# Performance work log

Hardware: AMD Instinct MI355X
Metric: run time of the kernel (lower is better)

The kernel has to match this reference:

```python
import jax, jax.numpy as jnp
import numpy as np

N_OSC = 256
N_LAYERS = 4
STEPS = 10
DT = 0.1
B = 1024
D_IN = 512
D_OUT = 128


def setup_inputs() -> dict:
    key = jax.random.key(0)
    ks = jax.random.split(key, 12)
    n = N_OSC

    def rn(k, shape, s=1.0):
        return jax.random.normal(k, shape, jnp.float32) * s

    K = rn(ks[0], (N_LAYERS, n, n), 0.1)
    K = (K + jnp.swapaxes(K, -1, -2)) / 2  # symmetric init as in torch
    return {
        "x": rn(ks[1], (B, D_IN)),
        "enc_W1": rn(ks[2], (D_IN, 2 * n), 0.02), "enc_b1": jnp.zeros((2 * n,), jnp.float32),
        "enc_W2": rn(ks[3], (2 * n, n), 0.02), "enc_b2": jnp.zeros((n,), jnp.float32),
        "K": K,
        "omega": rn(ks[4], (N_LAYERS, n), 0.1),
        "K_global": jnp.full((N_LAYERS,), 0.5, jnp.float32),
        "op_strength": jnp.full((6,), 0.5, jnp.float32),
        "exchange_logits": rn(ks[5], (n, n), 0.1),
        "catalyze_freq": rn(ks[6], (n,), 0.1),
        "sel_W1": rn(ks[7], (n + 2, 64), 0.05), "sel_b1": jnp.zeros((64,), jnp.float32),
        "sel_W2": rn(ks[8], (64, 6), 0.05), "sel_b2": jnp.zeros((6,), jnp.float32),
        "dec_W1": rn(ks[9], (2 * n, 2 * D_OUT), 0.02), "dec_b1": jnp.zeros((2 * D_OUT,), jnp.float32),
        "dec_W2": rn(ks[10], (2 * D_OUT, D_OUT), 0.02), "dec_b2": jnp.zeros((D_OUT,), jnp.float32),
        "z_momentum": jnp.float32(0.1),
        "z_decay": jnp.float32(0.05),
    }


def _kuramoto_layer(theta, K, omega, K_global):
    n = theta.shape[-1]

    def step(th, _):
        diff = th[:, None, :] - th[:, :, None]          # [B, i, j] = theta_j - theta_i
        coupling = jnp.sum(K * jnp.sin(diff), axis=-1)  # reduce over j -> [B, n]
        th_new = th + DT * (omega + (K_global / n) * coupling)
        th_new = jnp.arctan2(jnp.sin(th_new), jnp.cos(th_new))  # wrap to (-pi, pi]
        return th_new, None

    theta, _ = jax.lax.scan(jax.checkpoint(step), theta, None, length=STEPS)
    cm = jnp.mean(jnp.cos(theta), axis=-1)
    sm = jnp.mean(jnp.sin(theta), axis=-1)
    return theta, jnp.sqrt(cm * cm + sm * sm)  # Kuramoto order parameter r


def _soft_permutation(logits):
    P = logits
    for _ in range(5):  # Sinkhorn normalization in log space
        P = P - jax.nn.logsumexp(P, axis=-1, keepdims=True)
        P = P - jax.nn.logsumexp(P, axis=-2, keepdims=True)
    return jnp.exp(P)


def _forward(x, enc_W1, enc_b1, enc_W2, enc_b2, K, omega, K_global,
             op_strength, exchange_logits, catalyze_freq,
             sel_W1, sel_b1, sel_W2, sel_b2, dec_W1, dec_b1, dec_W2, dec_b2,
             z_momentum, z_decay):
    n = N_OSC
    # input encoding -> initial phases in (-pi, pi)
    h = jax.nn.gelu(x @ enc_W1 + enc_b1, approximate=False)
    theta = jnp.tanh(h @ enc_W2 + enc_b2) * jnp.pi

    z = jnp.float32(0.1)
    P = _soft_permutation(exchange_logits)
    k_mult = jnp.float32(1.0)              # AMPLIFY/CONTAIN carry to next layer
    om_add = jnp.zeros((n,), theta.dtype)  # CATALYZE carry to next layer

    for li in range(N_LAYERS):
        theta, r = _kuramoto_layer(theta, K[li] * k_mult, omega[li] + om_add, K_global[li])
        # z-coordinate attractor update: dz = mom*(r_mean - z) - decay*(z - 0.5)
        dz = z_momentum * (jnp.mean(r) - z) - z_decay * (z - 0.5)
        z = jnp.clip(z + 0.01 * dz, 0.0, 1.0)
        # APL operator selection from [theta, coherence, z]
        feat = jnp.concatenate(
            [theta, r[:, None], jnp.broadcast_to(z, (theta.shape[0], 1))], axis=-1)
        logits = jax.nn.gelu(feat @ sel_W1 + sel_b1, approximate=False) @ sel_W2 + sel_b2
        op = jnp.argmax(jnp.mean(logits, axis=0))
        strength = op_strength[op] * r[:, None]  # coherence-modulated strength
        sm_ = jnp.mean(strength)
        # apply operator: phase mods now, K/omega mods carried into next layer
        noise = jax.random.normal(jax.random.fold_in(jax.random.key(42), li),
                                  theta.shape, theta.dtype)
        theta = jnp.where(op == 3, theta @ P,                                # EXCHANGE
                          jnp.where(op == 4, theta + noise * strength * 0.2,  # INHIBIT
                                    theta))
        k_mult = jnp.where(op == 1, 1.0 + sm_ * 0.5,        # AMPLIFY
                           jnp.where(op == 2, 1.0 - sm_ * 0.3, 1.0))  # CONTAIN
        om_add = jnp.where(op == 5, catalyze_freq * sm_,    # CATALYZE
                           jnp.zeros_like(catalyze_freq))

    # decode from (cos, sin) phase embedding
    emb = jnp.concatenate([jnp.cos(theta), jnp.sin(theta)], axis=-1)  # [B, 2n]
    out = jax.nn.gelu(emb @ dec_W1 + dec_b1, approximate=False) @ dec_W2 + dec_b2
    return out


def reference(x, enc_W1, enc_b1, enc_W2, enc_b2, K, omega, K_global,
              op_strength, exchange_logits, catalyze_freq,
              sel_W1, sel_b1, sel_W2, sel_b2, dec_W1, dec_b1, dec_W2, dec_b2,
              z_momentum, z_decay):
    return _forward(x, enc_W1, enc_b1, enc_W2, enc_b2, K, omega, K_global,
                    op_strength, exchange_logits, catalyze_freq,
                    sel_W1, sel_b1, sel_W2, sel_b2, dec_W1, dec_b1, dec_W2, dec_b2,
                    z_momentum, z_decay)
```

## Files before the change

kernel.cpp:

```cpp
#include <hip/hip_runtime.h>
#include <hip/hip_fp16.h>
#include <math.h>

#define DT_F 0.1f

#define SC_Z     0
#define SC_RMEAN 1
#define SC_KMULT 2
#define SC_OP    3
#define SC_OPSTR 4
#define SC_SM    5

typedef __attribute__((ext_vector_type(8))) short short8;
typedef __attribute__((ext_vector_type(4))) float f32x4;


__device__ __forceinline__ float gelu_f(float x) {
    return 0.5f * x * (1.0f + erff(x * 0.7071067811865475f));
}

__device__ __forceinline__ unsigned short f2bf_rne(float f) {
    union { float f; unsigned u; } v; v.f = f;
    unsigned x = v.u;
    unsigned r = x + 0x7fffu + ((x >> 16) & 1u);
    return (unsigned short)(r >> 16);
}

__device__ __forceinline__ unsigned rotl32(unsigned v, int d) {
    return (v << d) | (v >> (32 - d));
}

__device__ __forceinline__ void threefry2x32(unsigned k0, unsigned k1,
                                             unsigned x0, unsigned x1,
                                             unsigned& o0, unsigned& o1) {
    unsigned k2 = k0 ^ k1 ^ 0x1BD11BDAu;
    x0 += k0; x1 += k1;
    const int r0[4] = {13, 15, 26, 6};
    const int r1[4] = {17, 29, 16, 24};
#pragma unroll
    for (int g = 0; g < 5; ++g) {
        const int* R = (g & 1) ? r1 : r0;
#pragma unroll
        for (int q = 0; q < 4; ++q) { x0 += x1; x1 = rotl32(x1, R[q]); x1 ^= x0; }
        unsigned a, b;
        switch (g) {
            case 0:  a = k1; b = k2 + 1u; break;
            case 1:  a = k2; b = k0 + 2u; break;
            case 2:  a = k0; b = k1 + 3u; break;
            case 3:  a = k1; b = k2 + 4u; break;
            default: a = k2; b = k0 + 5u; break;
        }
        x0 += a; x1 += b;
    }
    o0 = x0; o1 = x1;
}

__device__ __forceinline__ float erfinv_xla(float x) {
    float w = -log1pf(-x * x);
    float p;
    if (w < 5.0f) {
        w -= 2.5f;
        p = 2.81022636e-08f;
        p = fmaf(p, w, 3.43273939e-07f);
        p = fmaf(p, w, -3.5233877e-06f);
        p = fmaf(p, w, -4.39150654e-06f);
        p = fmaf(p, w, 0.00021858087f);
        p = fmaf(p, w, -0.00125372503f);
        p = fmaf(p, w, -0.00417768164f);
        p = fmaf(p, w, 0.246640727f);
        p = fmaf(p, w, 1.50140941f);
    } else {
        w = sqrtf(w) - 3.0f;
        p = -0.000200214257f;
        p = fmaf(p, w, 0.000100950558f);
        p = fmaf(p, w, 0.00134934322f);
        p = fmaf(p, w, -0.00367342844f);
        p = fmaf(p, w, 0.00573950773f);
        p = fmaf(p, w, -0.0076224613f);
        p = fmaf(p, w, 0.00943887047f);
        p = fmaf(p, w, 1.00167406f);
        p = fmaf(p, w, 2.83297682f);
    }
    return p * x;
}

__device__ __forceinline__ float jax_normal_elem(unsigned fk0, unsigned fk1, unsigned flat) {
    const unsigned HALF = 131072u;
    unsigned idx = (flat < HALF) ? flat : (flat - HALF);
    unsigned o0, o1;
    threefry2x32(fk0, fk1, idx, idx + HALF, o0, o1);
    unsigned bits = (flat < HALF) ? o0 : o1;
    float f = __uint_as_float((bits >> 9) | 0x3F800000u) - 1.0f;
    const float LO = __uint_as_float(0xBF7FFFFFu);
    float u = fmaxf(LO, fmaf(f, 2.0f, LO));
    return 1.41421356237f * erfinv_xla(u);
}


__global__ __launch_bounds__(256) void prep_wt_kernel(
    const float* __restrict__ W1, const float* __restrict__ W2,
    const float* __restrict__ W3, const float* __restrict__ W4,
    unsigned short* __restrict__ T1, unsigned short* __restrict__ T2,
    unsigned short* __restrict__ T3, unsigned short* __restrict__ T4)
{
    __shared__ float tile[64][65];
    int b = blockIdx.x;
    const float* W; unsigned short* T; int K, N, kt, nt;
    if (b < 64)       { W = W1; T = T1; K = 512; N = 512; kt = b >> 3; nt = b & 7; }
    else if (b < 96)  { b -= 64;  W = W2; T = T2; K = 512; N = 256; kt = b >> 2; nt = b & 3; }
    else if (b < 128) { b -= 96;  W = W3; T = T3; K = 512; N = 256; kt = b >> 2; nt = b & 3; }
    else              { b -= 128; W = W4; T = T4; K = 256; N = 128; kt = b >> 1; nt = b & 1; }
    const int k0 = kt * 64, n0 = nt * 64;
    const int t = threadIdx.x;

#pragma unroll
    for (int i = 0; i < 4; ++i) {
        int r = (t >> 4) + i * 16;
        int c = (t & 15) * 4;
        float4 v = *reinterpret_cast<const float4*>(&W[(k0 + r) * N + n0 + c]);
        tile[r][c] = v.x; tile[r][c + 1] = v.y; tile[r][c + 2] = v.z; tile[r][c + 3] = v.w;
    }
    __syncthreads();
#pragma unroll
    for (int i = 0; i < 4; ++i) {
        int nn = (t >> 4) + i * 16;
        int kc = (t & 15) * 4;
        ushort4 o;
        o.x = f2bf_rne(tile[kc + 0][nn]);
        o.y = f2bf_rne(tile[kc + 1][nn]);
        o.z = f2bf_rne(tile[kc + 2][nn]);
        o.w = f2bf_rne(tile[kc + 3][nn]);
        *reinterpret_cast<ushort4*>(&T[(n0 + nn) * K + k0 + kc]) = o;
    }
}


template <int ACT, int KF, bool EMB>
__global__ __launch_bounds__(256) void gemm_mfma_kernel(
    const float* __restrict__ A,
    const unsigned short* __restrict__ Wt,
    const float* __restrict__ bias,
    float* __restrict__ C, int N)
{
    constexpr int STR = KF + 8;
    __shared__ __align__(16) unsigned short A_s[64 * STR];
    __shared__ __align__(16) unsigned short B_s[64 * STR];
    const int tid = threadIdx.x;
    const int m_base = blockIdx.y * 64;
    const int n_base = blockIdx.x * 64;

    {
        constexpr int ITERS = 64 * KF / 2048;
#pragma unroll
        for (int c = 0; c < ITERS; ++c) {
            const int f = c * 2048 + tid * 8;
            const int row = f / KF, k = f % KF;
            float4 a0, a1;
            if (EMB) {
                const int kk = k & 255;
                a0 = *reinterpret_cast<const float4*>(&A[(m_base + row) * 256 + kk]);
                a1 = *reinterpret_cast<const float4*>(&A[(m_base + row) * 256 + kk + 4]);
                if (k < 256) {
                    a0.x = __cosf(a0.x); a0.y = __cosf(a0.y); a0.z = __cosf(a0.z); a0.w = __cosf(a0.w);
                    a1.x = __cosf(a1.x); a1.y = __cosf(a1.y); a1.z = __cosf(a1.z); a1.w = __cosf(a1.w);
                } else {
                    a0.x = __sinf(a0.x); a0.y = __sinf(a0.y); a0.z = __sinf(a0.z); a0.w = __sinf(a0.w);
                    a1.x = __sinf(a1.x); a1.y = __sinf(a1.y); a1.z = __sinf(a1.z); a1.w = __sinf(a1.w);
                }
            } else {
                a0 = *reinterpret_cast<const float4*>(&A[(m_base + row) * KF + k]);
                a1 = *reinterpret_cast<const float4*>(&A[(m_base + row) * KF + k + 4]);
            }
            short8 v;
            v[0] = (short)f2bf_rne(a0.x); v[1] = (short)f2bf_rne(a0.y);
            v[2] = (short)f2bf_rne(a0.z); v[3] = (short)f2bf_rne(a0.w);
            v[4] = (short)f2bf_rne(a1.x); v[5] = (short)f2bf_rne(a1.y);
            v[6] = (short)f2bf_rne(a1.z); v[7] = (short)f2bf_rne(a1.w);
            *reinterpret_cast<short8*>(&A_s[row * STR + k]) = v;
        }
    }
    {
        constexpr int ITERS = 64 * KF / 2048;
#pragma unroll
        for (int c = 0; c < ITERS; ++c) {
            const int f = c * 2048 + tid * 8;
            const int n = f / KF, k = f % KF;
            short8 v = *reinterpret_cast<const short8*>(&Wt[(n_base + n) * KF + k]);
            *reinterpret_cast<short8*>(&B_s[n * STR + k]) = v;
        }
    }
    __syncthreads();

    const int l = tid & 63, w = tid >> 6;
    const int lo = l & 15, hi = l >> 4;

    f32x4 acc0 = {0.f, 0.f, 0.f, 0.f};
    f32x4 acc1 = {0.f, 0.f, 0.f, 0.f};
    f32x4 acc2 = {0.f, 0.f, 0.f, 0.f};
    f32x4 acc3 = {0.f, 0.f, 0.f, 0.f};
#pragma unroll
    for (int kc = 0; kc < KF / 32; ++kc) {
        short8 af = *reinterpret_cast<const short8*>(&A_s[(w * 16 + lo) * STR + kc * 32 + hi * 8]);
        short8 b0 = *reinterpret_cast<const short8*>(&B_s[(0 * 16 + lo) * STR + kc * 32 + hi * 8]);
        short8 b1 = *reinterpret_cast<const short8*>(&B_s[(1 * 16 + lo) * STR + kc * 32 + hi * 8]);
        short8 b2 = *reinterpret_cast<const short8*>(&B_s[(2 * 16 + lo) * STR + kc * 32 + hi * 8]);
        short8 b3 = *reinterpret_cast<const short8*>(&B_s[(3 * 16 + lo) * STR + kc * 32 + hi * 8]);
        acc0 = __builtin_amdgcn_mfma_f32_16x16x32_bf16(af, b0, acc0, 0, 0, 0);
        acc1 = __builtin_amdgcn_mfma_f32_16x16x32_bf16(af, b1, acc1, 0, 0, 0);
        acc2 = __builtin_amdgcn_mfma_f32_16x16x32_bf16(af, b2, acc2, 0, 0, 0);
        acc3 = __builtin_amdgcn_mfma_f32_16x16x32_bf16(af, b3, acc3, 0, 0, 0);
    }

#pragma unroll
    for (int nf = 0; nf < 4; ++nf) {
        const f32x4 a = (nf == 0) ? acc0 : (nf == 1) ? acc1 : (nf == 2) ? acc2 : acc3;
        const int n = n_base + nf * 16 + lo;
        const float bv = bias[n];
#pragma unroll
        for (int q = 0; q < 4; ++q) {
            const int m = m_base + w * 16 + hi * 4 + q;
            float v = a[q] + bv;
            if (ACT == 1) v = gelu_f(v);
            else if (ACT == 2) v = tanhf(v) * 3.14159274101257324f;
            C[m * N + n] = v;
        }
    }
}


__global__ __launch_bounds__(1024) void sinkhorn_kernel(const float* __restrict__ logits,
                                                        float* __restrict__ P,
                                                        float* __restrict__ scal,
                                                        float* __restrict__ om_add) {
    __shared__ __align__(16) __half Eh[256][260];
    __shared__ float a[256], b[256];
    __shared__ float part[8][256];
    const int t = threadIdx.x;

    if (t < 8) {
        float val = 0.0f;
        if (t == SC_Z) val = 0.1f;
        if (t == SC_KMULT) val = 1.0f;
        scal[t] = val;
    }
    if (t < 256) { om_add[t] = 0.0f; b[t] = 1.0f; }

    {
        const int r = t >> 2, c0 = (t & 3) * 64;
#pragma unroll
        for (int j = 0; j < 64; j += 4) {
            float4 x4 = *reinterpret_cast<const float4*>(&logits[r * 256 + c0 + j]);
            __half2 h01 = __floats2half2_rn(__expf(x4.x), __expf(x4.y));
            __half2 h23 = __floats2half2_rn(__expf(x4.z), __expf(x4.w));
            *reinterpret_cast<__half2*>(&Eh[r][c0 + j])     = h01;
            *reinterpret_cast<__half2*>(&Eh[r][c0 + j + 2]) = h23;
        }
    }
    __syncthreads();

    for (int it = 0; it < 5; ++it) {
        {
            const int i = t & 255, q = t >> 8;
            float s0 = 0.f, s1 = 0.f, s2 = 0.f, s3 = 0.f;
#pragma unroll
            for (int j0 = 0; j0 < 64; j0 += 4) {
                float2 e4 = *reinterpret_cast<const float2*>(&Eh[i][q * 64 + j0]);
                const __half2* hp = reinterpret_cast<const __half2*>(&e4);
                float2 f01 = __half22float2(hp[0]);
                float2 f23 = __half22float2(hp[1]);
                float4 bv = *reinterpret_cast<const float4*>(&b[q * 64 + j0]);
                s0 = fmaf(f01.x, bv.x, s0);
                s1 = fmaf(f01.y, bv.y, s1);
                s2 = fmaf(f23.x, bv.z, s2);
                s3 = fmaf(f23.y, bv.w, s3);
            }
            part[q][i] = (s0 + s1) + (s2 + s3);
        }
        __syncthreads();
        if (t < 256) a[t] = 1.0f / (part[0][t] + part[1][t] + part[2][t] + part[3][t]);
        __syncthreads();
        {
            const int jp = t & 127, seg = t >> 7;
            float s0 = 0.f, s1 = 0.f;
#pragma unroll
            for (int i0 = 0; i0 < 32; i0 += 4) {
                float4 av = *reinterpret_cast<const float4*>(&a[seg * 32 + i0]);
                __half2 e0 = *reinterpret_cast<const __half2*>(&Eh[seg * 32 + i0 + 0][2 * jp]);
                __half2 e1 = *reinterpret_cast<const __half2*>(&Eh[seg * 32 + i0 + 1][2 * jp]);
                __half2 e2 = *reinterpret_cast<const __half2*>(&Eh[seg * 32 + i0 + 2][2 * jp]);
                __half2 e3 = *reinterpret_cast<const __half2*>(&Eh[seg * 32 + i0 + 3][2 * jp]);
                float2 f0 = __half22float2(e0), f1 = __half22float2(e1);
                float2 f2 = __half22float2(e2), f3 = __half22float2(e3);
                s0 = fmaf(f0.x, av.x, s0); s1 = fmaf(f0.y, av.x, s1);
                s0 = fmaf(f1.x, av.y, s0); s1 = fmaf(f1.y, av.y, s1);
                s0 = fmaf(f2.x, av.z, s0); s1 = fmaf(f2.y, av.z, s1);
                s0 = fmaf(f3.x, av.w, s0); s1 = fmaf(f3.y, av.w, s1);
            }
            part[seg][2 * jp]     = s0;
            part[seg][2 * jp + 1] = s1;
        }
        __syncthreads();
        if (t < 256) {
            float s = ((part[0][t] + part[1][t]) + (part[2][t] + part[3][t]))
                    + ((part[4][t] + part[5][t]) + (part[6][t] + part[7][t]));
            b[t] = 1.0f / s;
        }
        __syncthreads();
    }

    {
        const int r = t >> 2, c0 = (t & 3) * 64;
        const float ar = a[r];
#pragma unroll
        for (int j = 0; j < 64; j += 4) {
            float2 e4 = *reinterpret_cast<const float2*>(&Eh[r][c0 + j]);
            const __half2* hp = reinterpret_cast<const __half2*>(&e4);
            float2 f01 = __half22float2(hp[0]);
            float2 f23 = __half22float2(hp[1]);
            float4 bv = *reinterpret_cast<const float4*>(&b[c0 + j]);
            float4 o;
            o.x = f01.x * ar * bv.x;
            o.y = f01.y * ar * bv.y;
            o.z = f23.x * ar * bv.z;
            o.w = f23.y * ar * bv.w;
            *reinterpret_cast<float4*>(&P[r * 256 + c0 + j]) = o;
        }
    }
}


__global__ __launch_bounds__(512) void kuramoto_mfma_kernel(
    float* __restrict__ theta,
    const float* __restrict__ Kl,
    const float* __restrict__ omega_l,
    const float* __restrict__ Kg_p,
    const float* __restrict__ scal,
    const float* __restrict__ om_add,
    float* __restrict__ r_out,
    float* __restrict__ rpart,
    const float* __restrict__ P,
    int li)
{
    __shared__ __align__(16) unsigned short s_lds[2][16][264];
    __shared__ __align__(16) unsigned short c_lds[2][16][264];
    __shared__ __align__(16) float th_lds[16][260];
    __shared__ float rp_s[16][128];
    __shared__ float rp_c[16][128];
    __shared__ float red_s[16][32];
    __shared__ float red_c[16][32];
    __shared__ float rloc[16];

    const int tid = threadIdx.x;
    const int l  = tid & 63;
    const int w  = tid >> 6;
    const int lo = l & 15;
    const int hi = l >> 4;
    const int cb = w * 32;
    const int r0 = blockIdx.x * 16;

    const float gk = Kg_p[0] * (1.0f / 256.0f) * scal[SC_KMULT];
    const int op_prev = (int)scal[SC_OP];

    {
        const int row = tid >> 5;
        const int c0 = (tid & 31) * 8;
        float4 a = *reinterpret_cast<const float4*>(&theta[(r0 + row) * 256 + c0]);
        float4 b = *reinterpret_cast<const float4*>(&theta[(r0 + row) * 256 + c0 + 4]);
        *reinterpret_cast<float4*>(&th_lds[row][c0])     = a;
        *reinterpret_cast<float4*>(&th_lds[row][c0 + 4]) = b;
    }

    short8 kfrag[8][2];
#pragma unroll
    for (int nf = 0; nf < 2; ++nf) {
        const int col = cb + nf * 16 + lo;
        const float* krow = Kl + col * 256;
#pragma unroll
        for (int ks = 0; ks < 8; ++ks) {
            const int kb = ks * 32 + hi * 8;
            float4 k0 = *reinterpret_cast<const float4*>(&krow[kb]);
            float4 k1 = *reinterpret_cast<const float4*>(&krow[kb + 4]);
            short8 f;
            f[0] = (short)f2bf_rne(k0.x); f[1] = (short)f2bf_rne(k0.y);
            f[2] = (short)f2bf_rne(k0.z); f[3] = (short)f2bf_rne(k0.w);
            f[4] = (short)f2bf_rne(k1.x); f[5] = (short)f2bf_rne(k1.y);
            f[6] = (short)f2bf_rne(k1.z); f[7] = (short)f2bf_rne(k1.w);
            kfrag[ks][nf] = f;
        }
    }
    __syncthreads();

    float t[2][4];
    if (op_prev == 3) {
        float acc[2][4] = {};
        for (int j = 0; j < 256; ++j) {
            float p0 = P[j * 256 + cb + lo];
            float p1 = P[j * 256 + cb + 16 + lo];
#pragma unroll
            for (int q = 0; q < 4; ++q) {
                float tv = th_lds[hi * 4 + q][j];
                acc[0][q] = fmaf(tv, p0, acc[0][q]);
                acc[1][q] = fmaf(tv, p1, acc[1][q]);
            }
        }
#pragma unroll
        for (int nf = 0; nf < 2; ++nf)
#pragma unroll
            for (int q = 0; q < 4; ++q) t[nf][q] = acc[nf][q];
    } else {
#pragma unroll
        for (int nf = 0; nf < 2; ++nf)
#pragma unroll
            for (int q = 0; q < 4; ++q)
                t[nf][q] = th_lds[hi * 4 + q][cb + nf * 16 + lo];
        if (op_prev == 4) {
            unsigned fk0, fk1;
            threefry2x32(0u, 42u, 0u, (unsigned)(li - 1), fk0, fk1);
            const float opv = scal[SC_OPSTR];
#pragma unroll
            for (int nf = 0; nf < 2; ++nf)
#pragma unroll
                for (int q = 0; q < 4; ++q) {
                    const int row = hi * 4 + q;
                    const int col = cb + nf * 16 + lo;
                    unsigned flat = (unsigned)((r0 + row) * 256 + col);
                    float nz = jax_normal_elem(fk0, fk1, flat);
                    t[nf][q] += nz * opv * r_out[r0 + row] * 0.2f;
                }
        }
    }

    float si[2][4], ci[2][4];
    float om[2];
#pragma unroll
    for (int nf = 0; nf < 2; ++nf) {
        const int col = cb + nf * 16 + lo;
        om[nf] = omega_l[col] + om_add[col];
#pragma unroll
        for (int q = 0; q < 4; ++q) {
            const int row = hi * 4 + q;
            float sv, cv;
            __sincosf(t[nf][q], &sv, &cv);
            si[nf][q] = sv; ci[nf][q] = cv;
            s_lds[0][row][col] = f2bf_rne(sv);
            c_lds[0][row][col] = f2bf_rne(cv);
        }
    }
    __syncthreads();

    int cur = 0;
    for (int s = 0; s < 10; ++s) {
        f32x4 accS0 = {0.f, 0.f, 0.f, 0.f};
        f32x4 accS1 = {0.f, 0.f, 0.f, 0.f};
        f32x4 accC0 = {0.f, 0.f, 0.f, 0.f};
        f32x4 accC1 = {0.f, 0.f, 0.f, 0.f};
#pragma unroll
        for (int ks = 0; ks < 8; ++ks) {
            short8 aS = *reinterpret_cast<const short8*>(&s_lds[cur][lo][ks * 32 + hi * 8]);
            short8 aC = *reinterpret_cast<const short8*>(&c_lds[cur][lo][ks * 32 + hi * 8]);
            accS0 = __builtin_amdgcn_mfma_f32_16x16x32_bf16(aS, kfrag[ks][0], accS0, 0, 0, 0);
            accS1 = __builtin_amdgcn_mfma_f32_16x16x32_bf16(aS, kfrag[ks][1], accS1, 0, 0, 0);
            accC0 = __builtin_amdgcn_mfma_f32_16x16x32_bf16(aC, kfrag[ks][0], accC0, 0, 0, 0);
            accC1 = __builtin_amdgcn_mfma_f32_16x16x32_bf16(aC, kfrag[ks][1], accC1, 0, 0, 0);
        }
        const int nxt = cur ^ 1;
#pragma unroll
        for (int nf = 0; nf < 2; ++nf) {
#pragma unroll
            for (int q = 0; q < 4; ++q) {
                float aS = (nf == 0) ? accS0[q] : accS1[q];
                float aC = (nf == 0) ? accC0[q] : accC1[q];
                float coup = ci[nf][q] * aS - si[nf][q] * aC;
                float tn = t[nf][q] + DT_F * (om[nf] + gk * coup);
                t[nf][q] = tn;
                float sv, cv;
                __sincosf(tn, &sv, &cv);
                si[nf][q] = sv; ci[nf][q] = cv;
                const int row = hi * 4 + q;
                const int col = cb + nf * 16 + lo;
                s_lds[nxt][row][col] = f2bf_rne(sv);
                c_lds[nxt][row][col] = f2bf_rne(cv);
            }
        }
        __syncthreads();
        cur = nxt;
    }

#pragma unroll
    for (int q = 0; q < 4; ++q) {
        const int row = hi * 4 + q;
        rp_s[row][w * 16 + lo] = si[0][q] + si[1][q];
        rp_c[row][w * 16 + lo] = ci[0][q] + ci[1][q];
    }
#pragma unroll
    for (int nf = 0; nf < 2; ++nf) {
#pragma unroll
        for (int q = 0; q < 4; ++q) {
            const int row = hi * 4 + q;
            const int col = cb + nf * 16 + lo;
            theta[(r0 + row) * 256 + col] = atan2f(si[nf][q], ci[nf][q]);
        }
    }
    __syncthreads();

    {
        const int row = tid >> 5;
        const int i = tid & 31;
        float ssum = rp_s[row][i] + rp_s[row][i + 32] + rp_s[row][i + 64] + rp_s[row][i + 96];
        float csum = rp_c[row][i] + rp_c[row][i + 32] + rp_c[row][i + 64] + rp_c[row][i + 96];
        red_s[row][i] = ssum;
        red_c[row][i] = csum;
        __syncthreads();
#pragma unroll
        for (int off = 16; off > 0; off >>= 1) {
            if (i < off) {
                red_s[row][i] += red_s[row][i + off];
                red_c[row][i] += red_c[row][i + off];
            }
            __syncthreads();
        }
        if (i == 0) {
            float sm = red_s[row][0] * (1.0f / 256.0f);
            float cm = red_c[row][0] * (1.0f / 256.0f);
            float rv = sqrtf(cm * cm + sm * sm);
            r_out[r0 + row] = rv;
            rloc[row] = rv;
        }
        __syncthreads();
        if (tid == 0) {
            float s = 0.0f;
#pragma unroll
            for (int rr = 0; rr < 16; ++rr) s += rloc[rr];
            rpart[blockIdx.x] = s;
        }
    }
}


__global__ __launch_bounds__(256) void sel_partial_kernel(const float* __restrict__ theta,
                                                          const float* __restrict__ rbuf,
                                                          const float* __restrict__ rpart,
                                                          const float* __restrict__ scal,
                                                          const float* __restrict__ W1,
                                                          const float* __restrict__ b1,
                                                          const float* __restrict__ zm_p,
                                                          const float* __restrict__ zd_p,
                                                          float* __restrict__ partial) {
    __shared__ float Wt[64][261];
    __shared__ float th_s[4][256];
    __shared__ float gl[4][64];
    __shared__ float s_z;
    const int t = threadIdx.x;
    const int h = t & 63;
    const int rr = t >> 6;
    const int blk = blockIdx.x;

    if (t < 64) {
        float s = rpart[t];
#pragma unroll
        for (int off = 32; off > 0; off >>= 1) s += __shfl_down(s, off);
        if (t == 0) {
            float rmean = s * (1.0f / 1024.0f);
            float zp = scal[SC_Z];
            float dz = (*zm_p) * (rmean - zp) - (*zd_p) * (zp - 0.5f);
            float zn = zp + 0.01f * dz;
            s_z = fminf(fmaxf(zn, 0.0f), 1.0f);
        }
    }

    for (int idx = t; idx < 258 * 64; idx += 256)
        Wt[idx & 63][idx >> 6] = W1[idx];

    {
        const int c0 = h * 4;
        float4 v = *reinterpret_cast<const float4*>(&theta[(blk * 4 + rr) * 256 + c0]);
        *reinterpret_cast<float4*>(&th_s[rr][c0]) = v;
    }
    __syncthreads();

    const float z = s_z;
    float d0 = 0.f, d1 = 0.f, d2 = 0.f, d3 = 0.f;
#pragma unroll 4
    for (int k0 = 0; k0 < 256; k0 += 4) {
        float4 tv = *reinterpret_cast<const float4*>(&th_s[rr][k0]);
        d0 = fmaf(tv.x, Wt[h][k0 + 0], d0);
        d1 = fmaf(tv.y, Wt[h][k0 + 1], d1);
        d2 = fmaf(tv.z, Wt[h][k0 + 2], d2);
        d3 = fmaf(tv.w, Wt[h][k0 + 3], d3);
    }
    float full = (d0 + d1) + (d2 + d3) + b1[h]
               + rbuf[blk * 4 + rr] * Wt[h][256] + z * Wt[h][257];
    gl[rr][h] = gelu_f(full);
    __syncthreads();
    if (t < 64) partial[blk * 64 + t] = ((gl[0][t] + gl[1][t]) + gl[2][t]) + gl[3][t];
}


__global__ __launch_bounds__(256) void op_finalize_kernel(const float* __restrict__ partial,
                                                          const float* __restrict__ W2,
                                                          const float* __restrict__ b2,
                                                          const float* __restrict__ opstr,
                                                          const float* __restrict__ cf,
                                                          const float* __restrict__ rpart,
                                                          const float* __restrict__ zm_p,
                                                          const float* __restrict__ zd_p,
                                                          float* __restrict__ scal,
                                                          float* __restrict__ om_add) {
    __shared__ float red[4][64];
    __shared__ float hbar[64];
    __shared__ float lg[6];
    __shared__ float s_rmean;
    __shared__ float s_sm;
    __shared__ int s_op;
    const int t = threadIdx.x;
    const int h = t & 63;
    const int q = t >> 6;

    if (t < 64) {
        float s = rpart[t];
#pragma unroll
        for (int off = 32; off > 0; off >>= 1) s += __shfl_down(s, off);
        if (t == 0) s_rmean = s * (1.0f / 1024.0f);
    }

    float s = 0.0f;
#pragma unroll 8
    for (int blk = q * 64; blk < q * 64 + 64; ++blk) s += partial[blk * 64 + h];
    red[q][h] = s;
    __syncthreads();
    if (t < 64) hbar[t] = (red[0][t] + red[1][t] + red[2][t] + red[3][t]) * (1.0f / 1024.0f);
    __syncthreads();
    if (t < 6) {
        float l = b2[t];
        for (int hh = 0; hh < 64; ++hh) l = fmaf(hbar[hh], W2[hh * 6 + t], l);
        lg[t] = l;
    }
    __syncthreads();
    if (t == 0) {
        float rmean = s_rmean;
        float zp = scal[SC_Z];
        float dz = (*zm_p) * (rmean - zp) - (*zd_p) * (zp - 0.5f);
        float zn = zp + 0.01f * dz;
        zn = fminf(fmaxf(zn, 0.0f), 1.0f);
        scal[SC_Z] = zn;
        scal[SC_RMEAN] = rmean;

        float best = -1e30f;
        int op = 0;
#pragma unroll
        for (int o = 0; o < 6; ++o) {
            if (lg[o] > best) { best = lg[o]; op = o; }
        }
        float sm = opstr[op] * rmean;
        scal[SC_OP] = (float)op;
        scal[SC_OPSTR] = opstr[op];
        scal[SC_SM] = sm;
        scal[SC_KMULT] = (op == 1) ? (1.0f + sm * 0.5f)
                        : (op == 2) ? (1.0f - sm * 0.3f) : 1.0f;
        s_sm = sm;
        s_op = op;
    }
    __syncthreads();
    om_add[t] = (s_op == 5) ? cf[t] * s_sm : 0.0f;
}


__global__ __launch_bounds__(256) void apply_op_kernel(float* __restrict__ theta,
                                                       const float* __restrict__ P,
                                                       const float* __restrict__ r,
                                                       const float* __restrict__ scal,
                                                       int li) {
    __shared__ float th[8][256];
    const int op = (int)scal[SC_OP];
    const int i = threadIdx.x;
    const int b0 = blockIdx.x * 8;

    if (op == 3) {
#pragma unroll
        for (int rr = 0; rr < 8; ++rr) th[rr][i] = theta[(b0 + rr) * 256 + i];
        __syncthreads();
        float acc[8] = {0.f, 0.f, 0.f, 0.f, 0.f, 0.f, 0.f, 0.f};
        for (int j = 0; j < 256; ++j) {
            float pv = P[j * 256 + i];
#pragma unroll
            for (int rr = 0; rr < 8; ++rr) acc[rr] = fmaf(th[rr][j], pv, acc[rr]);
        }
#pragma unroll
        for (int rr = 0; rr < 8; ++rr) theta[(b0 + rr) * 256 + i] = acc[rr];
    } else if (op == 4) {
        unsigned fk0, fk1;
        threefry2x32(0u, 42u, 0u, (unsigned)li, fk0, fk1);
        const float opv = scal[SC_OPSTR];
#pragma unroll
        for (int rr = 0; rr < 8; ++rr) {
            int b = b0 + rr;
            unsigned flat = (unsigned)(b * 256 + i);
            float nz = jax_normal_elem(fk0, fk1, flat);
            float strength = opv * r[b];
            theta[b * 256 + i] += nz * strength * 0.2f;
        }
    }
}


extern "C" void kernel_launch(void* const* d_in, const int* in_sizes, int n_in,
                              void* d_out, int out_size, void* d_ws, size_t ws_size,
                              hipStream_t stream) {
    const float* x     = (const float*)d_in[0];
    const float* eW1   = (const float*)d_in[1];
    const float* eb1   = (const float*)d_in[2];
    const float* eW2   = (const float*)d_in[3];
    const float* eb2   = (const float*)d_in[4];
    const float* K     = (const float*)d_in[5];
    const float* omega = (const float*)d_in[6];
    const float* Kg    = (const float*)d_in[7];
    const float* opstr = (const float*)d_in[8];
    const float* exlog = (const float*)d_in[9];
    const float* cfreq = (const float*)d_in[10];
    const float* sW1   = (const float*)d_in[11];
    const float* sb1   = (const float*)d_in[12];
    const float* sW2   = (const float*)d_in[13];
    const float* sb2   = (const float*)d_in[14];
    const float* dW1   = (const float*)d_in[15];
    const float* db1   = (const float*)d_in[16];
    const float* dW2   = (const float*)d_in[17];
    const float* db2   = (const float*)d_in[18];
    const float* zm    = (const float*)d_in[19];
    const float* zd    = (const float*)d_in[20];
    float* out = (float*)d_out;

    float* ws      = (float*)d_ws;
    float* P       = ws;
    float* theta   = P + 65536;
    float* h       = theta + 262144;
    float* dh      = h + 524288;
    float* rbuf    = dh + 262144;
    float* scal    = rbuf + 1024;
    float* om_add  = scal + 8;
    float* partial = om_add + 256;
    float* rpart   = partial + 16384;
    unsigned short* W1t = (unsigned short*)(rpart + 64);
    unsigned short* W2t = (unsigned short*)(rpart + 64 + 131072);
    unsigned short* W3t = (unsigned short*)(rpart + 64 + 131072 + 65536);
    unsigned short* W4t = (unsigned short*)(rpart + 64 + 131072 + 65536 + 65536);

    prep_wt_kernel<<<136, 256, 0, stream>>>(eW1, eW2, dW1, dW2, W1t, W2t, W3t, W4t);
    sinkhorn_kernel<<<1, 1024, 0, stream>>>(exlog, P, scal, om_add);

    gemm_mfma_kernel<1, 512, false><<<dim3(8, 16), 256, 0, stream>>>(x, W1t, eb1, h, 512);
    gemm_mfma_kernel<2, 512, false><<<dim3(4, 16), 256, 0, stream>>>(h, W2t, eb2, theta, 256);

    for (int li = 0; li < 4; ++li) {
        kuramoto_mfma_kernel<<<64, 512, 0, stream>>>(theta, K + li * 65536, omega + li * 256,
                                                     Kg + li, scal, om_add, rbuf, rpart, P, li);
        sel_partial_kernel<<<256, 256, 0, stream>>>(theta, rbuf, rpart, scal, sW1, sb1,
                                                    zm, zd, partial);
        op_finalize_kernel<<<1, 256, 0, stream>>>(partial, sW2, sb2, opstr, cfreq, rpart,
                                                  zm, zd, scal, om_add);
    }

    apply_op_kernel<<<128, 256, 0, stream>>>(theta, P, rbuf, scal, 3);
    gemm_mfma_kernel<1, 512, true><<<dim3(4, 16), 256, 0, stream>>>(theta, W3t, db1, dh, 256);
    gemm_mfma_kernel<0, 256, false><<<dim3(2, 16), 256, 0, stream>>>(dh, W4t, db2, out, 128);

    (void)in_sizes; (void)n_in; (void)out_size; (void)ws_size;
}
```

Before: 204.9 us.

## Fold op-selection finalize into next Kuramoto layer and apply kernel

Removes the single-block op_finalize kernel launched after every layer. Each Kuramoto block and the final apply_op block now redundantly reduce the selector partials, compute the logits and argmax, and derive the coupling multiplier and frequency offset locally. r buffers are double-buffered so the previous layer's values can be read while the current ones are written. This saves four launches and their serialization gaps, at the cost of duplicated small reductions in every block.

Result: no change. 202.5 us (-1.1%).

```diff
diff --git a/kernel.cpp b/kernel.cpp
--- a/kernel.cpp
+++ b/kernel.cpp
@@ -3,13 +3,6 @@
 #include <math.h>
 
 #define DT_F 0.1f
-
-#define SC_Z     0
-#define SC_RMEAN 1
-#define SC_KMULT 2
-#define SC_OP    3
-#define SC_OPSTR 4
-#define SC_SM    5
 
 typedef __attribute__((ext_vector_type(8))) short short8;
 typedef __attribute__((ext_vector_type(4))) float f32x4;
@@ -230,20 +223,14 @@
 
 __global__ __launch_bounds__(1024) void sinkhorn_kernel(const float* __restrict__ logits,
                                                         float* __restrict__ P,
-                                                        float* __restrict__ scal,
-                                                        float* __restrict__ om_add) {
+                                                        float* __restrict__ zbuf) {
     __shared__ __align__(16) __half Eh[256][260];
     __shared__ float a[256], b[256];
     __shared__ float part[8][256];
     const int t = threadIdx.x;
 
-    if (t < 8) {
-        float val = 0.0f;
-        if (t == SC_Z) val = 0.1f;
-        if (t == SC_KMULT) val = 1.0f;
-        scal[t] = val;
-    }
-    if (t < 256) { om_add[t] = 0.0f; b[t] = 1.0f; }
+    if (t == 0) zbuf[0] = 0.1f;
+    if (t < 256) b[t] = 1.0f;
 
     {
         const int r = t >> 2, c0 = (t & 3) * 64;
@@ -334,11 +321,19 @@
     const float* __restrict__ Kl,
     const float* __restrict__ omega_l,
     const float* __restrict__ Kg_p,
-    const float* __restrict__ scal,
-    const float* __restrict__ om_add,
-    float* __restrict__ r_out,
-    float* __restrict__ rpart,
     const float* __restrict__ P,
+    const float* __restrict__ rpart_prev,
+    float* __restrict__ rpart_cur,
+    const float* __restrict__ rbuf_prev,
+    float* __restrict__ rbuf_cur,
+    const float* __restrict__ partial,
+    const float* __restrict__ sW2,
+    const float* __restrict__ sb2,
+    const float* __restrict__ opstr,
+    const float* __restrict__ cf,
+    const float* __restrict__ zm_p,
+    const float* __restrict__ zd_p,
+    float* __restrict__ zbuf,
     int li)
 {
     __shared__ __align__(16) unsigned short s_lds[2][16][264];
@@ -349,6 +344,10 @@
     __shared__ float red_s[16][32];
     __shared__ float red_c[16][32];
     __shared__ float rloc[16];
+    __shared__ float red4[4][64];
+    __shared__ float hbar_s[64];
+    __shared__ float lgs[6];
+    __shared__ float s_rmean;
 
     const int tid = threadIdx.x;
     const int l  = tid & 63;
@@ -358,9 +357,6 @@
     const int cb = w * 32;
     const int r0 = blockIdx.x * 16;
 
-    const float gk = Kg_p[0] * (1.0f / 256.0f) * scal[SC_KMULT];
-    const int op_prev = (int)scal[SC_OP];
-
     {
         const int row = tid >> 5;
         const int c0 = (tid & 31) * 8;
@@ -368,6 +364,52 @@
         float4 b = *reinterpret_cast<const float4*>(&theta[(r0 + row) * 256 + c0 + 4]);
         *reinterpret_cast<float4*>(&th_lds[row][c0])     = a;
         *reinterpret_cast<float4*>(&th_lds[row][c0 + 4]) = b;
+    }
+
+    int op_c = 0;
+    float sm_c = 0.0f, km_c = 1.0f, opv_c = 0.0f;
+    if (li > 0) {
+        if (tid < 64) {
+            float s = rpart_prev[tid];
+#pragma unroll
+            for (int off = 32; off > 0; off >>= 1) s += __shfl_down(s, off);
+            if (tid == 0) s_rmean = s * (1.0f / 1024.0f);
+        }
+        if (tid < 256) {
+            const int h = tid & 63, q = tid >> 6;
+            float s = 0.0f;
+#pragma unroll 8
+            for (int bb = q * 64; bb < q * 64 + 64; ++bb) s += partial[bb * 64 + h];
+            red4[q][h] = s;
+        }
+        __syncthreads();
+        if (tid < 64)
+            hbar_s[tid] = (red4[0][tid] + red4[1][tid] + red4[2][tid] + red4[3][tid])
+                        * (1.0f / 1024.0f);
+        __syncthreads();
+        if (tid < 6) {
+            float lv = sb2[tid];
+            for (int hh = 0; hh < 64; ++hh) lv = fmaf(hbar_s[hh], sW2[hh * 6 + tid], lv);
+            lgs[tid] = lv;
+        }
+        __syncthreads();
+        {
+            float best = -1e30f;
+#pragma unroll
+            for (int o = 0; o < 6; ++o) {
+                if (lgs[o] > best) { best = lgs[o]; op_c = o; }
+            }
+            const float rmean = s_rmean;
+            opv_c = opstr[op_c];
+            sm_c  = opv_c * rmean;
+            km_c  = (op_c == 1) ? (1.0f + sm_c * 0.5f)
+                  : (op_c == 2) ? (1.0f - sm_c * 0.3f) : 1.0f;
+            if (tid == 0) {
+                float zp = zbuf[li - 1];
+                float dz = (*zm_p) * (rmean - zp) - (*zd_p) * (zp - 0.5f);
+                zbuf[li] = fminf(fmaxf(zp + 0.01f * dz, 0.0f), 1.0f);
+            }
+        }
     }
 
     short8 kfrag[8][2];
@@ -390,8 +432,10 @@
     }
     __syncthreads();
 
+    const float gk = Kg_p[0] * (1.0f / 256.0f) * km_c;
+
     float t[2][4];
-    if (op_prev == 3) {
+    if (op_c == 3) {
         float acc[2][4] = {};
         for (int j = 0; j < 256; ++j) {
             float p0 = P[j * 256 + cb + lo];
@@ -413,10 +457,9 @@
 #pragma unroll
             for (int q = 0; q < 4; ++q)
                 t[nf][q] = th_lds[hi * 4 + q][cb + nf * 16 + lo];
-        if (op_prev == 4) {
+        if (op_c == 4) {
             unsigned fk0, fk1;
             threefry2x32(0u, 42u, 0u, (unsigned)(li - 1), fk0, fk1);
-            const float opv = scal[SC_OPSTR];
 #pragma unroll
             for (int nf = 0; nf < 2; ++nf)
 #pragma unroll
@@ -425,7 +468,7 @@
                     const int col = cb + nf * 16 + lo;
                     unsigned flat = (unsigned)((r0 + row) * 256 + col);
                     float nz = jax_normal_elem(fk0, fk1, flat);
-                    t[nf][q] += nz * opv * r_out[r0 + row] * 0.2f;
+                    t[nf][q] += nz * opv_c * rbuf_prev[r0 + row] * 0.2f;
                 }
         }
     }
@@ -435,7 +478,7 @@
 #pragma unroll
     for (int nf = 0; nf < 2; ++nf) {
         const int col = cb + nf * 16 + lo;
-        om[nf] = omega_l[col] + om_add[col];
+        om[nf] = omega_l[col] + ((op_c == 5) ? cf[col] * sm_c : 0.0f);
 #pragma unroll
         for (int q = 0; q < 4; ++q) {
             const int row = hi * 4 + q;
@@ -523,7 +566,7 @@
             float sm = red_s[row][0] * (1.0f / 256.0f);
             float cm = red_c[row][0] * (1.0f / 256.0f);
             float rv = sqrtf(cm * cm + sm * sm);
-            r_out[r0 + row] = rv;
+            rbuf_cur[r0 + row] = rv;
             rloc[row] = rv;
         }
         __syncthreads();
@@ -531,7 +574,7 @@
             float s = 0.0f;
 #pragma unroll
             for (int rr = 0; rr < 16; ++rr) s += rloc[rr];
-            rpart[blockIdx.x] = s;
+            rpart_cur[blockIdx.x] = s;
         }
     }
 }
@@ -540,12 +583,13 @@
 __global__ __launch_bounds__(256) void sel_partial_kernel(const float* __restrict__ theta,
                                                           const float* __restrict__ rbuf,
                                                           const float* __restrict__ rpart,
-                                                          const float* __restrict__ scal,
+                                                          const float* __restrict__ zbuf,
                                                           const float* __restrict__ W1,
                                                           const float* __restrict__ b1,
                                                           const float* __restrict__ zm_p,
                                                           const float* __restrict__ zd_p,
-                                                          float* __restrict__ partial) {
+                                                          float* __restrict__ partial,
+                                                          int li) {
     __shared__ float Wt[64][261];
     __shared__ float th_s[4][256];
     __shared__ float gl[4][64];
@@ -561,7 +605,7 @@
         for (int off = 32; off > 0; off >>= 1) s += __shfl_down(s, off);
         if (t == 0) {
             float rmean = s * (1.0f / 1024.0f);
-            float zp = scal[SC_Z];
+            float zp = zbuf[li];
             float dz = (*zm_p) * (rmean - zp) - (*zd_p) * (zp - 0.5f);
             float zn = zp + 0.01f * dz;
             s_z = fminf(fmaxf(zn, 0.0f), 1.0f);
@@ -596,84 +640,55 @@
 }
 
 
-__global__ __launch_bounds__(256) void op_finalize_kernel(const float* __restrict__ partial,
-                                                          const float* __restrict__ W2,
-                                                          const float* __restrict__ b2,
-                                                          const float* __restrict__ opstr,
-                                                          const float* __restrict__ cf,
-                                                          const float* __restrict__ rpart,
-                                                          const float* __restrict__ zm_p,
-                                                          const float* __restrict__ zd_p,
-                                                          float* __restrict__ scal,
-                                                          float* __restrict__ om_add) {
-    __shared__ float red[4][64];
-    __shared__ float hbar[64];
-    __shared__ float lg[6];
-    __shared__ float s_rmean;
-    __shared__ float s_sm;
-    __shared__ int s_op;
-    const int t = threadIdx.x;
-    const int h = t & 63;
-    const int q = t >> 6;
-
-    if (t < 64) {
-        float s = rpart[t];
-#pragma unroll
-        for (int off = 32; off > 0; off >>= 1) s += __shfl_down(s, off);
-        if (t == 0) s_rmean = s * (1.0f / 1024.0f);
-    }
-
-    float s = 0.0f;
-#pragma unroll 8
-    for (int blk = q * 64; blk < q * 64 + 64; ++blk) s += partial[blk * 64 + h];
-    red[q][h] = s;
-    __syncthreads();
-    if (t < 64) hbar[t] = (red[0][t] + red[1][t] + red[2][t] + red[3][t]) * (1.0f / 1024.0f);
-    __syncthreads();
-    if (t < 6) {
-        float l = b2[t];
-        for (int hh = 0; hh < 64; ++hh) l = fmaf(hbar[hh], W2[hh * 6 + t], l);
-        lg[t] = l;
-    }
-    __syncthreads();
-    if (t == 0) {
-        float rmean = s_rmean;
-        float zp = scal[SC_Z];
-        float dz = (*zm_p) * (rmean - zp) - (*zd_p) * (zp - 0.5f);
-        float zn = zp + 0.01f * dz;
-        zn = fminf(fmaxf(zn, 0.0f), 1.0f);
-        scal[SC_Z] = zn;
-        scal[SC_RMEAN] = rmean;
-
-        float best = -1e30f;
-        int op = 0;
-#pragma unroll
-        for (int o = 0; o < 6; ++o) {
-            if (lg[o] > best) { best = lg[o]; op = o; }
-        }
-        float sm = opstr[op] * rmean;
-        scal[SC_OP] = (float)op;
-        scal[SC_OPSTR] = opstr[op];
-        scal[SC_SM] = sm;
-        scal[SC_KMULT] = (op == 1) ? (1.0f + sm * 0.5f)
-                        : (op == 2) ? (1.0f - sm * 0.3f) : 1.0f;
-        s_sm = sm;
-        s_op = op;
-    }
-    __syncthreads();
-    om_add[t] = (s_op == 5) ? cf[t] * s_sm : 0.0f;
-}
-
-
 __global__ __launch_bounds__(256) void apply_op_kernel(float* __restrict__ theta,
                                                        const float* __restrict__ P,
                                                        const float* __restrict__ r,
-                                                       const float* __restrict__ scal,
+                                                       const float* __restrict__ rpart,
+                                                       const float* __restrict__ partial,
+                                                       const float* __restrict__ sW2,
+                                                       const float* __restrict__ sb2,
+                                                       const float* __restrict__ opstr,
                                                        int li) {
     __shared__ float th[8][256];
-    const int op = (int)scal[SC_OP];
+    __shared__ float red4[4][64];
+    __shared__ float hbar_s[64];
+    __shared__ float lgs[6];
+    __shared__ float s_rmean;
     const int i = threadIdx.x;
     const int b0 = blockIdx.x * 8;
+
+    if (i < 64) {
+        float s = rpart[i];
+#pragma unroll
+        for (int off = 32; off > 0; off >>= 1) s += __shfl_down(s, off);
+        if (i == 0) s_rmean = s * (1.0f / 1024.0f);
+    }
+    {
+        const int h = i & 63, q = i >> 6;
+        float s = 0.0f;
+#pragma unroll 8
+        for (int bb = q * 64; bb < q * 64 + 64; ++bb) s += partial[bb * 64 + h];
+        red4[q][h] = s;
+    }
+    __syncthreads();
+    if (i < 64)
+        hbar_s[i] = (red4[0][i] + red4[1][i] + red4[2][i] + red4[3][i]) * (1.0f / 1024.0f);
+    __syncthreads();
+    if (i < 6) {
+        float lv = sb2[i];
+        for (int hh = 0; hh < 64; ++hh) lv = fmaf(hbar_s[hh], sW2[hh * 6 + i], lv);
+        lgs[i] = lv;
+    }
+    __syncthreads();
+    int op = 0;
+    {
+        float best = -1e30f;
+#pragma unroll
+        for (int o = 0; o < 6; ++o) {
+            if (lgs[o] > best) { best = lgs[o]; op = o; }
+        }
+    }
+    const float opv = opstr[op];
 
     if (op == 3) {
 #pragma unroll
@@ -690,7 +705,6 @@
     } else if (op == 4) {
         unsigned fk0, fk1;
         threefry2x32(0u, 42u, 0u, (unsigned)li, fk0, fk1);
-        const float opv = scal[SC_OPSTR];
 #pragma unroll
         for (int rr = 0; rr < 8; ++rr) {
             int b = b0 + rr;
@@ -729,37 +743,40 @@
     const float* zd    = (const float*)d_in[20];
     float* out = (float*)d_out;
 
-    float* ws      = (float*)d_ws;
-    float* P       = ws;
-    float* theta   = P + 65536;
-    float* h       = theta + 262144;
-    float* dh      = h + 524288;
-    float* rbuf    = dh + 262144;
-    float* scal    = rbuf + 1024;
-    float* om_add  = scal + 8;
-    float* partial = om_add + 256;
-    float* rpart   = partial + 16384;
-    unsigned short* W1t = (unsigned short*)(rpart + 64);
-    unsigned short* W2t = (unsigned short*)(rpart + 64 + 131072);
-    unsigned short* W3t = (unsigned short*)(rpart + 64 + 131072 + 65536);
-    unsigned short* W4t = (unsigned short*)(rpart + 64 + 131072 + 65536 + 65536);
+    float* ws       = (float*)d_ws;
+    float* P        = ws;
+    float* theta    = P + 65536;
+    float* h        = theta + 262144;
+    float* dh       = h + 524288;
+    float* rbuf2    = dh + 262144;
+    float* rpart2   = rbuf2 + 2048;
+    float* partial  = rpart2 + 128;
+    float* zbuf     = partial + 16384;
+    unsigned short* W1t = (unsigned short*)(zbuf + 8);
+    unsigned short* W2t = W1t + 262144;
+    unsigned short* W3t = W2t + 131072;
+    unsigned short* W4t = W3t + 131072;
 
     prep_wt_kernel<<<136, 256, 0, stream>>>(eW1, eW2, dW1, dW2, W1t, W2t, W3t, W4t);
-    sinkhorn_kernel<<<1, 1024, 0, stream>>>(exlog, P, scal, om_add);
+    sinkhorn_kernel<<<1, 1024, 0, stream>>>(exlog, P, zbuf);
 
     gemm_mfma_kernel<1, 512, false><<<dim3(8, 16), 256, 0, stream>>>(x, W1t, eb1, h, 512);
     gemm_mfma_kernel<2, 512, false><<<dim3(4, 16), 256, 0, stream>>>(h, W2t, eb2, theta, 256);
 
     for (int li = 0; li < 4; ++li) {
-        kuramoto_mfma_kernel<<<64, 512, 0, stream>>>(theta, K + li * 65536, omega + li * 256,
-                                                     Kg + li, scal, om_add, rbuf, rpart, P, li);
-        sel_partial_kernel<<<256, 256, 0, stream>>>(theta, rbuf, rpart, scal, sW1, sb1,
-                                                    zm, zd, partial);
-        op_finalize_kernel<<<1, 256, 0, stream>>>(partial, sW2, sb2, opstr, cfreq, rpart,
-                                                  zm, zd, scal, om_add);
-    }
-
-    apply_op_kernel<<<128, 256, 0, stream>>>(theta, P, rbuf, scal, 3);
+        const int pc = li & 1, pp = (li - 1) & 1;
+        kuramoto_mfma_kernel<<<64, 512, 0, stream>>>(
+            theta, K + li * 65536, omega + li * 256, Kg + li, P,
+            rpart2 + pp * 64, rpart2 + pc * 64,
+            rbuf2 + pp * 1024, rbuf2 + pc * 1024,
+            partial, sW2, sb2, opstr, cfreq, zm, zd, zbuf, li);
+        sel_partial_kernel<<<256, 256, 0, stream>>>(
+            theta, rbuf2 + pc * 1024, rpart2 + pc * 64, zbuf,
+            sW1, sb1, zm, zd, partial, li);
+    }
+
+    apply_op_kernel<<<128, 256, 0, stream>>>(theta, P, rbuf2 + 1024, rpart2 + 64,
+                                             partial, sW2, sb2, opstr, 3);
     gemm_mfma_kernel<1, 512, true><<<dim3(4, 16), 256, 0, stream>>>(theta, W3t, db1, dh, 256);
     gemm_mfma_kernel<0, 256, false><<<dim3(2, 16), 256, 0, stream>>>(dh, W4t, db2, out, 128);
 
```
